# Optimization experiments

Hardware: AMD Instinct MI355X
Metric: run time of the kernel (lower is better)

## Reference

```python
import jax, jax.numpy as jnp
import numpy as np
from jax import lax

H = W = 1024            # input frame size
STRIDE = 16             # backbone total stride (4 stride-2 convs)
FH = FW = H // STRIDE   # 64x64 feature map
A = 3                   # anchors per cell
SIZES = (32.0, 64.0, 128.0)
K = 100                 # fixed NMS candidate count (jit-static)
SCORE_TH = 0.5          # kwargs['threshhold']
IOU_TH = 0.5
BORDER = 4              # draw_boxes border_size=4


def _conv(x, w, b, stride):
    y = lax.conv_general_dilated(x, w, (stride, stride), 'SAME',
                                 dimension_numbers=('NCHW', 'OIHW', 'NCHW'))
    return y + b[None, :, None, None]


def _anchors():
    ys, xs = jnp.meshgrid(jnp.arange(FH, dtype=jnp.float32),
                          jnp.arange(FW, dtype=jnp.float32), indexing='ij')
    cx = (xs + 0.5) * STRIDE
    cy = (ys + 0.5) * STRIDE
    sz = jnp.asarray(SIZES, dtype=jnp.float32)
    cx = jnp.broadcast_to(cx[:, :, None], (FH, FW, A))
    cy = jnp.broadcast_to(cy[:, :, None], (FH, FW, A))
    ww = jnp.broadcast_to(sz[None, None, :], (FH, FW, A))
    return jnp.stack([cx, cy, ww, ww], -1).reshape(-1, 4)  # [N,4] cx,cy,w,h


def _facenet(frame, w1, b1, w2, b2, w3, b3, w4, b4, wh, bh):
    x = jax.nn.relu(_conv(frame, w1, b1, 2))   # [1,32,512,512]
    x = jax.nn.relu(_conv(x, w2, b2, 2))       # [1,64,256,256]
    x = jax.nn.relu(_conv(x, w3, b3, 2))       # [1,128,128,128]
    x = jax.nn.relu(_conv(x, w4, b4, 2))       # [1,256,64,64]
    p = _conv(x, wh, bh, 1)                    # [1,A*5,64,64]
    p = p.reshape(A, 5, FH, FW).transpose(2, 3, 0, 1).reshape(-1, 5)  # [N,5]
    t, logit = p[:, :4], p[:, 4]
    a = _anchors()
    cx = a[:, 0] + t[:, 0] * a[:, 2]
    cy = a[:, 1] + t[:, 1] * a[:, 3]
    bw = a[:, 2] * jnp.exp(jnp.clip(t[:, 2], -4.0, 4.0))
    bhh = a[:, 3] * jnp.exp(jnp.clip(t[:, 3], -4.0, 4.0))
    boxes = jnp.stack([cx - bw * 0.5, cy - bhh * 0.5,
                       cx + bw * 0.5, cy + bhh * 0.5], -1)  # [N,4] xyxy
    scores = jax.nn.sigmoid(logit)             # [N]
    return boxes, scores


def _pairwise_iou(b):
    area = (b[:, 2] - b[:, 0]) * (b[:, 3] - b[:, 1])
    lt = jnp.maximum(b[:, None, :2], b[None, :, :2])
    rb = jnp.minimum(b[:, None, 2:], b[None, :, 2:])
    wh2 = jnp.clip(rb - lt, 0.0)
    inter = wh2[..., 0] * wh2[..., 1]
    return inter / (area[:, None] + area[None, :] - inter + 1e-9)


def _nms(boxes, scores):
    s = jnp.where(scores >= SCORE_TH, scores, -1.0)
    top, idx = lax.top_k(s, K)
    b = boxes[idx]                    # [K,4], score-sorted
    valid = top > 0.0
    ious = _pairwise_iou(b)           # [K,K]
    rng = jnp.arange(K)

    def body(i, keep):
        sup = (ious[i] > IOU_TH) & keep[i] & (rng > i)
        return keep & (~sup)

    keep = lax.fori_loop(0, K, body, valid)
    return b, keep


def _draw(frame, boxes, keep):
    x1 = jnp.clip(boxes[:, 0], 0.0, W)[:, None, None]
    y1 = jnp.clip(boxes[:, 1], 0.0, H)[:, None, None]
    x2 = jnp.clip(boxes[:, 2], 0.0, W)[:, None, None]
    y2 = jnp.clip(boxes[:, 3], 0.0, H)[:, None, None]
    ys = jnp.arange(H, dtype=jnp.float32)[None, :, None]
    xs = jnp.arange(W, dtype=jnp.float32)[None, None, :]
    inside = (ys >= y1) & (ys < y2) & (xs >= x1) & (xs < x2)
    inner = (ys >= y1 + BORDER) & (ys < y2 - BORDER) & \
            (xs >= x1 + BORDER) & (xs < x2 - BORDER)
    border = inside & (~inner) & keep[:, None, None]   # [K,H,W]
    mask = jnp.any(border, axis=0)                     # [H,W]
    red = jnp.array([1.0, 0.0, 0.0], dtype=frame.dtype)[None, :, None, None]
    return jnp.where(mask[None, None, :, :], red, frame)


def setup_inputs() -> dict:
    key = jax.random.key(0)
    ks = jax.random.split(key, 12)
    sc = 0.05
    return {
        'frame': jax.random.normal(ks[0], (1, 3, H, W), jnp.float32),
        'w1': jax.random.normal(ks[1], (32, 3, 3, 3), jnp.float32) * sc,
        'b1': jax.random.normal(ks[2], (32,), jnp.float32) * sc,
        'w2': jax.random.normal(ks[3], (64, 32, 3, 3), jnp.float32) * sc,
        'b2': jax.random.normal(ks[4], (64,), jnp.float32) * sc,
        'w3': jax.random.normal(ks[5], (128, 64, 3, 3), jnp.float32) * sc,
        'b3': jax.random.normal(ks[6], (128,), jnp.float32) * sc,
        'w4': jax.random.normal(ks[7], (256, 128, 3, 3), jnp.float32) * sc,
        'b4': jax.random.normal(ks[8], (256,), jnp.float32) * sc,
        'wh': jax.random.normal(ks[9], (A * 5, 256, 3, 3), jnp.float32) * sc,
        'bh': jax.random.normal(ks[10], (A * 5,), jnp.float32) * sc,
    }


def reference(frame, w1, b1, w2, b2, w3, b3, w4, b4, wh, bh):
    boxes, scores = _facenet(frame, w1, b1, w2, b2, w3, b3, w4, b4, wh, bh)
    kept_boxes, keep = _nms(boxes, scores)     # kwargs: use_nms=True, only_anchors=False
    im = _draw(frame, kept_boxes, keep)        # border_size=4, color='red'
    return im
```

## Files before the change

kernel.cpp:

```cpp
#include <hip/hip_runtime.h>


constexpr int KTOP  = 100;
constexpr int NANCH = 12288;

template<int CIN, int HIN, int WIN, int STRIDE, int PXT, int COB, int CICHUNK, bool FUSEOUT>
__global__ __launch_bounds__(256)
void convk(const float* __restrict__ in, const float* __restrict__ w,
           const float* __restrict__ bias, float* __restrict__ out, int CO)
{
    constexpr int HOUT = (STRIDE == 2) ? HIN / 2 : HIN;
    constexpr int WOUT = (STRIDE == 2) ? WIN / 2 : WIN;
    constexpr int NPX  = HOUT * WOUT;
    constexpr int GPR  = WOUT / PXT;
    constexpr int NCOL = (STRIDE == 2) ? 2 * PXT + 1 : PXT + 2;

    const int g   = blockIdx.x * 256 + threadIdx.x;
    const int oy  = g / GPR;
    const int oxb = (g - oy * GPR) * PXT;
    const int co0 = blockIdx.y * COB;
    const int ci0 = blockIdx.z * CICHUNK;

    float acc[COB][PXT];
#pragma unroll
    for (int c = 0; c < COB; ++c)
#pragma unroll
        for (int p = 0; p < PXT; ++p) acc[c][p] = 0.f;

    const int iy0 = oy * STRIDE - ((STRIDE == 1) ? 1 : 0);
    const int ixb = oxb * STRIDE - ((STRIDE == 1) ? 1 : 0);

    for (int ci = ci0; ci < ci0 + CICHUNK; ++ci) {
#pragma unroll
        for (int ky = 0; ky < 3; ++ky) {
            const int iy = iy0 + ky;
            const float* __restrict__ rp = in + ((size_t)ci * HIN + iy) * WIN;
            float c[NCOL];
            if (iy >= 0 && iy < HIN) {
                if constexpr (STRIDE == 2) {
                    const float4 q0 = *reinterpret_cast<const float4*>(rp + ixb);
                    const float4 q1 = *reinterpret_cast<const float4*>(rp + ixb + 4);
                    c[0] = q0.x; c[1] = q0.y; c[2] = q0.z; c[3] = q0.w;
                    c[4] = q1.x; c[5] = q1.y; c[6] = q1.z; c[7] = q1.w;
                    c[8] = (ixb + 8 < WIN) ? rp[ixb + 8] : 0.f;
                } else {
                    c[0] = (ixb >= 0) ? rp[ixb] : 0.f;
                    c[1] = rp[ixb + 1];
                    c[2] = (ixb + 2 < WIN) ? rp[ixb + 2] : 0.f;
                }
            } else {
#pragma unroll
                for (int k = 0; k < NCOL; ++k) c[k] = 0.f;
            }
#pragma unroll
            for (int co = 0; co < COB; ++co) {
                const float* __restrict__ wp = w + (((size_t)(co0 + co) * CIN + ci) * 3 + ky) * 3;
#pragma unroll
                for (int kx = 0; kx < 3; ++kx) {
                    const float wv = wp[kx];
#pragma unroll
                    for (int p = 0; p < PXT; ++p)
                        acc[co][p] = fmaf(c[STRIDE * p + kx], wv, acc[co][p]);
                }
            }
        }
    }

    const int obase = oy * WOUT + oxb;
#pragma unroll
    for (int co = 0; co < COB; ++co) {
        float r[PXT];
#pragma unroll
        for (int p = 0; p < PXT; ++p) {
            r[p] = FUSEOUT ? fmaxf(acc[co][p] + bias[co0 + co], 0.f) : acc[co][p];
        }
        float* __restrict__ op = FUSEOUT
            ? out + (size_t)(co0 + co) * NPX + obase
            : out + ((size_t)blockIdx.z * CO + co0 + co) * NPX + obase;
        if constexpr (PXT == 4) {
            float4 q; q.x = r[0]; q.y = r[1]; q.z = r[2]; q.w = r[3];
            *reinterpret_cast<float4*>(op) = q;
        } else {
#pragma unroll
            for (int p = 0; p < PXT; ++p) op[p] = r[p];
        }
    }
}

template<int NCHUNK, int NPX, bool RELU>
__global__ __launch_bounds__(256)
void reducek(const float* __restrict__ part, const float* __restrict__ bias,
             float* __restrict__ out, int CO)
{
    const int t = blockIdx.x * 256 + threadIdx.x;
    const int co = t / NPX, px = t - co * NPX;
    float s = 0.f;
#pragma unroll
    for (int c = 0; c < NCHUNK; ++c) s += part[((size_t)c * CO + co) * NPX + px];
    s += bias[co];
    out[(size_t)co * NPX + px] = RELU ? fmaxf(s, 0.f) : s;
}

__global__ void decode_kernel(const float* __restrict__ head,
                              float4* __restrict__ boxes,
                              unsigned long long* __restrict__ keys)
{
    const int i = blockIdx.x * 256 + threadIdx.x;
    const int a = i % 3;
    const int xy = i / 3;
    const int x = xy & 63, y = xy >> 6;
    const int px = y * 64 + x;

    const float t0 = head[(a * 5 + 0) * 4096 + px];
    const float t1 = head[(a * 5 + 1) * 4096 + px];
    const float t2 = head[(a * 5 + 2) * 4096 + px];
    const float t3 = head[(a * 5 + 3) * 4096 + px];
    const float lg = head[(a * 5 + 4) * 4096 + px];

    const float sz  = (a == 0) ? 32.f : (a == 1) ? 64.f : 128.f;
    const float cxa = (x + 0.5f) * 16.f;
    const float cya = (y + 0.5f) * 16.f;

    const float cx = __fadd_rn(cxa, __fmul_rn(t0, sz));
    const float cy = __fadd_rn(cya, __fmul_rn(t1, sz));
    const float bw = __fmul_rn(sz, expf(fminf(fmaxf(t2, -4.f), 4.f)));
    const float bh = __fmul_rn(sz, expf(fminf(fmaxf(t3, -4.f), 4.f)));
    const float hw = __fmul_rn(bw, 0.5f);
    const float hh = __fmul_rn(bh, 0.5f);

    float4 bb;
    bb.x = __fsub_rn(cx, hw);
    bb.y = __fsub_rn(cy, hh);
    bb.z = __fadd_rn(cx, hw);
    bb.w = __fadd_rn(cy, hh);
    boxes[i] = bb;

    const float score = 1.f / (1.f + expf(-lg));
    unsigned long long key = 0ull;
    if (score >= 0.5f) {
        key = ((unsigned long long)__float_as_uint(score) << 32)
            | (unsigned long long)(0xFFFFFFFFu - (unsigned)i);
    }
    keys[i] = key;
}

constexpr int JSPLIT = 16;
constexpr int JCHUNK = NANCH / JSPLIT;

__global__ __launch_bounds__(256)
void rank_kernel(const unsigned long long* __restrict__ keys,
                 int* __restrict__ rank)
{
    const int i = blockIdx.x * 256 + threadIdx.x;
    const unsigned long long ki = keys[i];
    const int lane = threadIdx.x & 63;
    const int jbase = blockIdx.y * JCHUNK;

    int cnt = 0;
    for (int g = 0; g < JCHUNK / 64; ++g) {
        const unsigned long long kj = keys[jbase + g * 64 + lane];
        const unsigned lo0 = (unsigned)kj;
        const unsigned hi0 = (unsigned)(kj >> 32);
#pragma unroll
        for (int l = 0; l < 64; ++l) {
            const unsigned lo = (unsigned)__builtin_amdgcn_readlane((int)lo0, l);
            const unsigned hi = (unsigned)__builtin_amdgcn_readlane((int)hi0, l);
            const unsigned long long kjj = ((unsigned long long)hi << 32) | lo;
            cnt += (kjj > ki) ? 1 : 0;
        }
    }
    if (cnt) atomicAdd(&rank[i], cnt);
}

__global__ void scatter_kernel(const unsigned long long* __restrict__ keys,
                               const int* __restrict__ rank,
                               const float4* __restrict__ boxes,
                               float4* __restrict__ selb, int* __restrict__ selv)
{
    const int i = blockIdx.x * 256 + threadIdx.x;
    if (keys[i] == 0ull) return;
    const int r = rank[i];
    if (r < KTOP) { selb[r] = boxes[i]; selv[r] = 1; }
}

__global__ __launch_bounds__(128)
void nms_kernel(const float4* __restrict__ selb, const int* __restrict__ selv,
                float4* __restrict__ drawb)
{
    __shared__ float bx1[KTOP], by1[KTOP], bx2[KTOP], by2[KTOP], ar[KTOP];
    __shared__ int kp[KTOP];
    const int t = threadIdx.x;
    if (t < KTOP) {
        const float4 b = selb[t];
        bx1[t] = b.x; by1[t] = b.y; bx2[t] = b.z; by2[t] = b.w;
        ar[t] = (b.z - b.x) * (b.w - b.y);
        kp[t] = selv[t];
    }
    __syncthreads();
    for (int i = 0; i < KTOP - 1; ++i) {
        if (t > i && t < KTOP) {
            if (kp[i] && kp[t]) {
                const float lx = fmaxf(bx1[i], bx1[t]);
                const float ly = fmaxf(by1[i], by1[t]);
                const float rx = fminf(bx2[i], bx2[t]);
                const float ry = fminf(by2[i], by2[t]);
                const float ww = fmaxf(rx - lx, 0.f);
                const float hh = fmaxf(ry - ly, 0.f);
                const float inter = ww * hh;
                const float iou = inter / (ar[i] + ar[t] - inter + 1e-9f);
                if (iou > 0.5f) kp[t] = 0;
            }
        }
        __syncthreads();
    }
    if (t < KTOP) {
        float4 d;
        if (kp[t]) {
            d.x = fminf(fmaxf(bx1[t], 0.f), 1024.f);
            d.y = fminf(fmaxf(by1[t], 0.f), 1024.f);
            d.z = fminf(fmaxf(bx2[t], 0.f), 1024.f);
            d.w = fminf(fmaxf(by2[t], 0.f), 1024.f);
        } else {
            d.x = 3e9f; d.y = 3e9f; d.z = -3e9f; d.w = -3e9f;
        }
        drawb[t] = d;
    }
}

__global__ __launch_bounds__(256)
void draw_kernel(const float* __restrict__ frame,
                 const float4* __restrict__ drawb, float* __restrict__ out)
{
    const int y = blockIdx.x >> 2;
    const int x = ((blockIdx.x & 3) << 8) + threadIdx.x;
    const float fy = (float)y, fx = (float)x;

    bool mask = false;
#pragma unroll 1
    for (int b = 0; b < KTOP; ++b) {
        const float4 d = drawb[b];
        if (fy >= d.y && fy < d.w) {
            const bool yinner = (fy >= d.y + 4.f) && (fy < d.w - 4.f);
            const bool xin    = (fx >= d.x) && (fx < d.z);
            const bool xinner = (fx >= d.x + 4.f) && (fx < d.z - 4.f);
            mask |= xin && !(yinner && xinner);
        }
    }
    const int p = y * 1024 + x;
    const float f0 = frame[p];
    const float f1 = frame[1048576 + p];
    const float f2 = frame[2097152 + p];
    out[p]           = mask ? 1.f : f0;
    out[1048576 + p] = mask ? 0.f : f1;
    out[2097152 + p] = mask ? 0.f : f2;
}

extern "C" void kernel_launch(void* const* d_in, const int* in_sizes, int n_in,
                              void* d_out, int out_size, void* d_ws, size_t ws_size,
                              hipStream_t stream)
{
    const float* frame = (const float*)d_in[0];
    const float* w1 = (const float*)d_in[1];  const float* b1 = (const float*)d_in[2];
    const float* w2 = (const float*)d_in[3];  const float* b2 = (const float*)d_in[4];
    const float* w3 = (const float*)d_in[5];  const float* b3 = (const float*)d_in[6];
    const float* w4 = (const float*)d_in[7];  const float* b4 = (const float*)d_in[8];
    const float* wh = (const float*)d_in[9];  const float* bh = (const float*)d_in[10];

    char* ws = (char*)d_ws;
    float* buf1  = (float*)ws;
    float* buf2  = (float*)(ws + 33554432);
    float* part3 = (float*)ws;
    float* buf3  = (float*)(ws + 16777216);
    float* part4 = (float*)ws;
    float* buf4  = (float*)(ws + 25165824);
    float* partH = (float*)ws;
    float* heado = (float*)(ws + 29360128);
    char*  B     = ws + 33554432;
    float4* boxes = (float4*)(B);
    unsigned long long* keys = (unsigned long long*)(B + 196608);
    int*    rankb = (int*)(B + 294912);
    int*    selv  = (int*)(B + 344064);
    float4* selb  = (float4*)(B + 344576);
    float4* drawb = (float4*)(B + 346176);
    float*  outp  = (float*)d_out;

    convk<3, 1024, 1024, 2, 4, 8, 3,  true ><<<dim3(256,  4, 1), 256, 0, stream>>>(frame, w1, b1, buf1, 32);
    convk<32,  512,  512, 2, 4, 4, 32, true ><<<dim3(64,  16, 1), 256, 0, stream>>>(buf1, w2, b2, buf2, 64);
    convk<64,  256,  256, 2, 4, 4, 32, false><<<dim3(16,  32, 2), 256, 0, stream>>>(buf2, w3, nullptr, part3, 128);
    reducek<2, 16384, true><<<8192, 256, 0, stream>>>(part3, b3, buf3, 128);
    convk<128, 128,  128, 2, 4, 4, 32, false><<<dim3(4,   64, 4), 256, 0, stream>>>(buf3, w4, nullptr, part4, 256);
    reducek<4, 4096, true><<<4096, 256, 0, stream>>>(part4, b4, buf4, 256);

    convk<256, 64, 64, 1, 1, 15, 4, false><<<dim3(16, 1, 64), 256, 0, stream>>>(buf4, wh, nullptr, partH, 15);
    reducek<64, 4096, false><<<240, 256, 0, stream>>>(partH, bh, heado, 15);

    hipMemsetAsync(rankb, 0, 49152 + 512, stream);

    decode_kernel<<<48, 256, 0, stream>>>(heado, boxes, keys);
    rank_kernel<<<dim3(48, JSPLIT), 256, 0, stream>>>(keys, rankb);
    scatter_kernel<<<48, 256, 0, stream>>>(keys, rankb, boxes, selb, selv);
    nms_kernel<<<1, 128, 0, stream>>>(selb, selv, drawb);
    draw_kernel<<<4096, 256, 0, stream>>>(frame, drawb, outp);
}
```

Before: 423.7 us.

## Split input channels more finely across conv layers and rebalance workspace layout

Conv1 now computes 2 output channels per block instead of 8, which gives 4x more blocks. Conv2 gains a split-K path over input channels with a separate reduce kernel, used when the workspace is large enough. Conv3 and conv4 double their channel-split count, and the inner channel loop is unrolled by 2. The aim is more parallelism and occupancy on early layers that had few blocks, paid for with larger partial-sum buffers, extra reduction traffic and an extra kernel launch. Workspace offsets are reorganized to fit the new buffers.

```diff
diff --git a/kernel.cpp b/kernel.cpp
--- a/kernel.cpp
+++ b/kernel.cpp
@@ -30,7 +30,9 @@
     const int iy0 = oy * STRIDE - ((STRIDE == 1) ? 1 : 0);
     const int ixb = oxb * STRIDE - ((STRIDE == 1) ? 1 : 0);
 
-    for (int ci = ci0; ci < ci0 + CICHUNK; ++ci) {
+#pragma unroll 2
+    for (int cii = 0; cii < CICHUNK; ++cii) {
+        const int ci = ci0 + cii;
 #pragma unroll
         for (int ky = 0; ky < 3; ++ky) {
             const int iy = iy0 + ky;
@@ -267,29 +269,40 @@
     const float* wh = (const float*)d_in[9];  const float* bh = (const float*)d_in[10];
 
     char* ws = (char*)d_ws;
+    const bool big = ws_size >= (size_t)70 * 1024 * 1024;
+
     float* buf1  = (float*)ws;
-    float* buf2  = (float*)(ws + 33554432);
-    float* part3 = (float*)ws;
-    float* buf3  = (float*)(ws + 16777216);
+    float* part2 = (float*)(ws + 33554432);
+    float* buf2  = big ? (float*)ws : (float*)(ws + 33554432);
+    float* part3 = big ? (float*)(ws + 16777216) : (float*)ws;
+    float* buf3  = big ? (float*)(ws + 50331648) : (float*)(ws + 33554432);
     float* part4 = (float*)ws;
-    float* buf4  = (float*)(ws + 25165824);
+    float* buf4  = big ? (float*)(ws + 33554432) : (float*)(ws + 41943040);
     float* partH = (float*)ws;
-    float* heado = (float*)(ws + 29360128);
-    char*  B     = ws + 33554432;
-    float4* boxes = (float4*)(B);
-    unsigned long long* keys = (unsigned long long*)(B + 196608);
-    int*    rankb = (int*)(B + 294912);
-    int*    selv  = (int*)(B + 344064);
-    float4* selb  = (float4*)(B + 344576);
-    float4* drawb = (float4*)(B + 346176);
+    float* heado = big ? (float*)(ws + 46137344) : (float*)(ws + 16777216);
+    char*  D     = big ? (ws + 47185920) : (ws + 17825792);
+    float4* boxes = (float4*)(D);
+    unsigned long long* keys = (unsigned long long*)(D + 196608);
+    int*    rankb = (int*)(D + 294912);
+    int*    selv  = (int*)(D + 344064);
+    float4* selb  = (float4*)(D + 344576);
+    float4* drawb = (float4*)(D + 346176);
     float*  outp  = (float*)d_out;
 
-    convk<3, 1024, 1024, 2, 4, 8, 3,  true ><<<dim3(256,  4, 1), 256, 0, stream>>>(frame, w1, b1, buf1, 32);
-    convk<32,  512,  512, 2, 4, 4, 32, true ><<<dim3(64,  16, 1), 256, 0, stream>>>(buf1, w2, b2, buf2, 64);
-    convk<64,  256,  256, 2, 4, 4, 32, false><<<dim3(16,  32, 2), 256, 0, stream>>>(buf2, w3, nullptr, part3, 128);
-    reducek<2, 16384, true><<<8192, 256, 0, stream>>>(part3, b3, buf3, 128);
-    convk<128, 128,  128, 2, 4, 4, 32, false><<<dim3(4,   64, 4), 256, 0, stream>>>(buf3, w4, nullptr, part4, 256);
-    reducek<4, 4096, true><<<4096, 256, 0, stream>>>(part4, b4, buf4, 256);
+    convk<3, 1024, 1024, 2, 4, 2, 3, true ><<<dim3(256, 16, 1), 256, 0, stream>>>(frame, w1, b1, buf1, 32);
+
+    if (big) {
+        convk<32, 512, 512, 2, 4, 4, 16, false><<<dim3(64, 16, 2), 256, 0, stream>>>(buf1, w2, nullptr, part2, 64);
+        reducek<2, 65536, true><<<16384, 256, 0, stream>>>(part2, b2, buf2, 64);
+    } else {
+        convk<32, 512, 512, 2, 4, 4, 32, true ><<<dim3(64, 16, 1), 256, 0, stream>>>(buf1, w2, b2, buf2, 64);
+    }
+
+    convk<64, 256, 256, 2, 4, 4, 16, false><<<dim3(16, 32, 4), 256, 0, stream>>>(buf2, w3, nullptr, part3, 128);
+    reducek<4, 16384, true><<<8192, 256, 0, stream>>>(part3, b3, buf3, 128);
+
+    convk<128, 128, 128, 2, 4, 4, 16, false><<<dim3(4, 64, 8), 256, 0, stream>>>(buf3, w4, nullptr, part4, 256);
+    reducek<8, 4096, true><<<4096, 256, 0, stream>>>(part4, b4, buf4, 256);
 
     convk<256, 64, 64, 1, 1, 15, 4, false><<<dim3(16, 1, 64), 256, 0, stream>>>(buf4, wh, nullptr, partH, 15);
     reducek<64, 4096, false><<<240, 256, 0, stream>>>(partH, bh, heado, 15);
```

Result: slower. 470.8 us (+11.1%).
